# Optimization experiments

Hardware: AMD Instinct MI355X
Metric: run time of the kernel (lower is better)

## Reference

```python
import jax, jax.numpy as jnp
import numpy as np

B, N, D, K = 256, 500000, 64, 100


def setup_inputs() -> dict:
    key = jax.random.key(0)
    k1, k2, k3 = jax.random.split(key, 3)
    query_embedding = jax.random.normal(k1, (B, D), dtype=jnp.float32)
    corpus = jax.random.normal(k2, (N, D), dtype=jnp.float32)
    corpus_id = jax.random.randint(k3, (N,), 0, 10_000_000).astype(jnp.int64)
    return {
        "query_embedding": query_embedding,
        "corpus": corpus,
        "corpus_id": corpus_id,
        "num_items": K,
    }


def reference(query_embedding, corpus, corpus_id, num_items):
    # Inner-product scores: [B, N]
    scores = jnp.matmul(query_embedding, corpus.T)
    # Top-k along the corpus axis (lax.top_k returns sorted descending,
    # matching torch.topk defaults): values [B, k], indices [B, k]
    inprod_scores, indices = jax.lax.top_k(scores, num_items)
    # Gather ids and embeddings of the neighbors
    item_ids = corpus_id[indices]          # [B, k]
    embeddings = corpus[indices]           # [B, k, D]
    return (item_ids, inprod_scores, embeddings)
```

## Files before the change

kernel.cpp:

```cpp
#include <hip/hip_runtime.h>
#include <math.h>

#define NQ      256
#define DIM     64
#define NCORPUS 500000
#define K       100
#define CAP     2048
#define ZTHRESH 3.0f

#define NSUB    16
#define SUBCAP  160
#define TILE    32
#define NTILES  (NCORPUS / TILE)
#define K1BLOCKS 1024

typedef __bf16 bf16x8 __attribute__((ext_vector_type(8)));
typedef float  f32x16 __attribute__((ext_vector_type(16)));

static __device__ __forceinline__ bf16x8 pack8(float4 a, float4 b) {
    bf16x8 r;
    r[0] = (__bf16)a.x; r[1] = (__bf16)a.y; r[2] = (__bf16)a.z; r[3] = (__bf16)a.w;
    r[4] = (__bf16)b.x; r[5] = (__bf16)b.y; r[6] = (__bf16)b.z; r[7] = (__bf16)b.w;
    return r;
}

__global__ void k0_setup(const float* __restrict__ q, int* __restrict__ cnt2,
                         float* __restrict__ t) {
    int b = threadIdx.x;
    const float4* qb = (const float4*)(q + b * DIM);
    float s = 0.f;
#pragma unroll
    for (int i = 0; i < DIM / 4; ++i) {
        float4 v = qb[i];
        s += v.x * v.x + v.y * v.y + v.z * v.z + v.w * v.w;
    }
    t[b] = ZTHRESH * sqrtf(s);
    for (int i = b; i < NQ * NSUB * 4; i += 256) cnt2[i] = 0;
}

__global__ __launch_bounds__(256, 4)
void k1_score_filter(const float* __restrict__ q, const float* __restrict__ c,
                     const float* __restrict__ t, int* __restrict__ cnt2,
                     int* __restrict__ cand2) {
    const int tid  = threadIdx.x;
    const int ln   = tid & 63;
    const int lm   = ln & 31;
    const int half = ln >> 5;

    __shared__ __align__(16) __bf16 qf[2048 * 8];

#pragma unroll
    for (int u = 0; u < 8; ++u) {
        const int ch = u * 256 + tid;
        const int ci = ch >> 8;
        const int cs = (ch >> 6) & 3;
        const int cl = ch & 63;
        const float* src =
            q + ((ci << 5) + (cl & 31)) * DIM + cs * 16 + ((cl >> 5) << 3);
        float4 a = *(const float4*)src;
        float4 b = *(const float4*)(src + 4);
        *(bf16x8*)(qf + (size_t)ch * 8) = pack8(a, b);
    }
    __syncthreads();

    float tq[8];
#pragma unroll
    for (int i = 0; i < 8; ++i) tq[i] = t[(i << 5) + lm];

    const f32x16 z16 = {0, 0, 0, 0, 0, 0, 0, 0, 0, 0, 0, 0, 0, 0, 0, 0};

    const int wid    = (blockIdx.x << 2) | (tid >> 6);
    const int stride = gridDim.x << 2;
    const int sub    = wid & (NSUB - 1);

    float4 st[8];
#define LOADC(tl)                                                             \
    {                                                                         \
        const float* gp = c + (size_t)((tl) * TILE + lm) * DIM + (half << 3); \
        _Pragma("unroll") for (int s = 0; s < 4; ++s) {                       \
            st[2 * s]     = *(const float4*)(gp + s * 16);                    \
            st[2 * s + 1] = *(const float4*)(gp + s * 16 + 4);                \
        }                                                                     \
    }
    LOADC(wid);

    for (int tl = wid; tl < NTILES; tl += stride) {
        float4 cur[8];
#pragma unroll
        for (int s = 0; s < 8; ++s) cur[s] = st[s];
        const int nx = tl + stride;
        if (nx < NTILES) LOADC(nx);
        bf16x8 af[4];
#pragma unroll
        for (int s = 0; s < 4; ++s) af[s] = pack8(cur[2 * s], cur[2 * s + 1]);

        for (int i = 0; i < 8; ++i) {
            const __bf16* bp = qf + ((size_t)(i << 2) * 64 + ln) * 8;
            bf16x8 b0 = *(const bf16x8*)(bp);
            bf16x8 b1 = *(const bf16x8*)(bp + 512);
            bf16x8 b2 = *(const bf16x8*)(bp + 1024);
            bf16x8 b3 = *(const bf16x8*)(bp + 1536);
            f32x16 acc;
            acc = __builtin_amdgcn_mfma_f32_32x32x16_bf16(af[0], b0, z16, 0, 0, 0);
            acc = __builtin_amdgcn_mfma_f32_32x32x16_bf16(af[1], b1, acc, 0, 0, 0);
            acc = __builtin_amdgcn_mfma_f32_32x32x16_bf16(af[2], b2, acc, 0, 0, 0);
            acc = __builtin_amdgcn_mfma_f32_32x32x16_bf16(af[3], b3, acc, 0, 0, 0);
            float mx = acc[0];
#pragma unroll
            for (int r = 1; r < 16; ++r) mx = fmaxf(mx, acc[r]);
            const float ti = tq[i];
            if (__any(mx > ti)) {
                const int qidx = (i << 5) + lm;
                const int rowb = tl * TILE + (half << 2);
#pragma unroll
                for (int r = 0; r < 16; ++r) {
                    if (acc[r] > ti) {
                        int slot = atomicAdd(&cnt2[(qidx * NSUB + sub) * 4], 1);
                        if (slot < SUBCAP)
                            cand2[(size_t)(qidx * NSUB + sub) * SUBCAP + slot] =
                                rowb + (r & 3) + ((r >> 2) << 3);
                    }
                }
            }
        }
    }
#undef LOADC
}

__global__ __launch_bounds__(512) void k2_select(
    const float* __restrict__ q, const float* __restrict__ c,
    const int* __restrict__ ids, const int* __restrict__ cnt2,
    const int* __restrict__ cand2, float* __restrict__ out) {
    const int b = blockIdx.x;
    const int tid = threadIdx.x;
    __shared__ double qd[DIM];
    __shared__ int pref[NSUB + 1];
    __shared__ int clist[CAP];
    __shared__ unsigned long long keys[CAP];
    __shared__ int sidx[K];

    if (tid < DIM) qd[tid] = (double)q[b * DIM + tid];
    if (tid == 0) {
        int a = 0;
        for (int s = 0; s < NSUB; ++s) {
            pref[s] = a;
            int cs = cnt2[(b * NSUB + s) * 4];
            if (cs > SUBCAP) cs = SUBCAP;
            a += cs;
            if (a > CAP) a = CAP;
        }
        pref[NSUB] = a;
    }
    __syncthreads();
#pragma unroll
    for (int s = 0; s < NSUB; ++s) {
        const int base = pref[s];
        const int cs = pref[s + 1] - base;
        for (int i = tid; i < cs; i += 512)
            clist[base + i] = cand2[(size_t)(b * NSUB + s) * SUBCAP + i];
    }
    __syncthreads();
    const int n = pref[NSUB];
    int p = 128;
    while (p < n) p <<= 1;

    for (int i = tid; i < p; i += 512) {
        unsigned long long key = 0ull;
        if (i < n) {
            const int idx = clist[i];
            const float4* cr = (const float4*)(c + (size_t)idx * DIM);
            double acc = 0.0;
#pragma unroll
            for (int d4 = 0; d4 < DIM / 4; ++d4) {
                float4 v = cr[d4];
                acc += qd[4 * d4 + 0] * (double)v.x;
                acc += qd[4 * d4 + 1] * (double)v.y;
                acc += qd[4 * d4 + 2] * (double)v.z;
                acc += qd[4 * d4 + 3] * (double)v.w;
            }
            const float sc = (float)acc;
            unsigned u = __float_as_uint(sc);
            u = (u & 0x80000000u) ? ~u : (u | 0x80000000u);
            key = ((unsigned long long)u << 32) | (unsigned)(~(unsigned)idx);
        }
        keys[i] = key;
    }
    __syncthreads();

    for (int kk = 2; kk <= p; kk <<= 1) {
        for (int j = kk >> 1; j > 0; j >>= 1) {
            for (int i = tid; i < p; i += 512) {
                const int l = i ^ j;
                if (l > i) {
                    const unsigned long long a = keys[i], bb = keys[l];
                    const bool desc = ((i & kk) == 0);
                    if (desc ? (a < bb) : (a > bb)) {
                        keys[i] = bb;
                        keys[l] = a;
                    }
                }
            }
            __syncthreads();
        }
    }

    if (tid < K) {
        const unsigned long long key = keys[tid];
        const unsigned uk = (unsigned)(key >> 32);
        const unsigned us = (uk & 0x80000000u) ? (uk & 0x7fffffffu) : ~uk;
        int idx = (int)(~(unsigned)(key & 0xffffffffu));
        if ((unsigned)idx >= NCORPUS) idx = 0;
        sidx[tid] = idx;
        out[b * K + tid] = (float)ids[idx];
        out[NQ * K + b * K + tid] = __uint_as_float(us);
    }
    __syncthreads();
    for (int e = tid; e < K * DIM; e += 512) {
        const int j = e >> 6;
        const int d = e & 63;
        out[2 * NQ * K + (size_t)b * K * DIM + e] = c[(size_t)sidx[j] * DIM + d];
    }
}

extern "C" void kernel_launch(void* const* d_in, const int* in_sizes, int n_in,
                              void* d_out, int out_size, void* d_ws,
                              size_t ws_size, hipStream_t stream) {
    const float* q = (const float*)d_in[0];
    const float* c = (const float*)d_in[1];
    const int* ids = (const int*)d_in[2];
    float* out = (float*)d_out;

    char* ws = (char*)d_ws;
    float* t   = (float*)ws;
    int* cnt2  = (int*)(ws + 4096);
    int* cand2 = (int*)(ws + 4096 + 65536);

    k0_setup<<<1, 256, 0, stream>>>(q, cnt2, t);
    k1_score_filter<<<K1BLOCKS, 256, 0, stream>>>(q, c, t, cnt2, cand2);
    k2_select<<<NQ, 512, 0, stream>>>(q, c, ids, cnt2, cand2, out);
}
```

Baseline: 270.3 us.

## Stage corpus tiles via async global-to-LDS triple buffering and batch candidate atomics

The scoring kernel now streams corpus tiles into a per-wave triple-buffered LDS region using global_load_lds with swizzled offsets and explicit vmcnt waits, replacing the register-held prefetch. Grid size drops to 256 blocks, and the occupancy hint is removed. Candidates are first appended to a per-wave LDS queue and flushed to the global per-query buckets at the end, which cuts global atomics during the main loop. The risks are lower occupancy from the large LDS footprint and silently dropped candidates if a wave's queue exceeds its capacity of 320.

```diff
diff --git a/kernel.cpp b/kernel.cpp
--- a/kernel.cpp
+++ b/kernel.cpp
@@ -1,5 +1,6 @@
 #include <hip/hip_runtime.h>
 #include <math.h>
+#include <stdint.h>
 
 #define NQ      256
 #define DIM     64
@@ -12,10 +13,16 @@
 #define SUBCAP  160
 #define TILE    32
 #define NTILES  (NCORPUS / TILE)
-#define K1BLOCKS 1024
+#define K1BLOCKS 256
+#define NWAVE1  (K1BLOCKS * 4)
+#define WQCAP   320
 
 typedef __bf16 bf16x8 __attribute__((ext_vector_type(8)));
 typedef float  f32x16 __attribute__((ext_vector_type(16)));
+typedef __attribute__((address_space(3))) unsigned       lds_u32;
+typedef const __attribute__((address_space(1))) unsigned glb_u32;
+
+#define WAITVM(N) __builtin_amdgcn_s_waitcnt(((N) & 0xF) | (((N) >> 4) << 14) | 0x0F70)
 
 static __device__ __forceinline__ bf16x8 pack8(float4 a, float4 b) {
     bf16x8 r;
@@ -38,7 +45,7 @@
     for (int i = b; i < NQ * NSUB * 4; i += 256) cnt2[i] = 0;
 }
 
-__global__ __launch_bounds__(256, 4)
+__global__ __launch_bounds__(256)
 void k1_score_filter(const float* __restrict__ q, const float* __restrict__ c,
                      const float* __restrict__ t, int* __restrict__ cnt2,
                      int* __restrict__ cand2) {
@@ -46,8 +53,14 @@
     const int ln   = tid & 63;
     const int lm   = ln & 31;
     const int half = ln >> 5;
+    const int wv   = tid >> 6;
 
     __shared__ __align__(16) __bf16 qf[2048 * 8];
+    __shared__ __align__(16) char   cbuf[4 * 3 * 8192];
+    __shared__ unsigned wq[4 * WQCAP];
+    __shared__ int wqc[4 * 16];
+
+    if (ln == 0) wqc[wv * 16] = 0;
 
 #pragma unroll
     for (int u = 0; u < 8; ++u) {
@@ -67,32 +80,64 @@
 #pragma unroll
     for (int i = 0; i < 8; ++i) tq[i] = t[(i << 5) + lm];
 
+    int offs[8];
+#pragma unroll
+    for (int g = 0; g < 8; ++g) {
+        int r = g * 4 + (ln >> 4);
+        int j = (ln & 15) ^ (r & 15);
+        offs[g] = r * 256 + j * 16;
+    }
+    int roff[8];
+#pragma unroll
+    for (int s = 0; s < 4; ++s) {
+        int c0 = s * 4 + half * 2;
+#pragma unroll
+        for (int tt = 0; tt < 2; ++tt)
+            roff[s * 2 + tt] = lm * 256 + ((((c0 + tt) ^ (lm & 15))) << 4);
+    }
+
+    char* cbase = cbuf + wv * 3 * 8192;
+    const int wid = (blockIdx.x << 2) | wv;
+    const int sub = wid & (NSUB - 1);
+
+    WAITVM(0);
+
+#define STAGE(tl, bi)                                                         \
+    {                                                                         \
+        const char* gb = (const char*)c + (size_t)(tl) * 8192;                \
+        char* lb = cbase + (bi) * 8192;                                       \
+        _Pragma("unroll") for (int g = 0; g < 8; ++g)                         \
+            __builtin_amdgcn_global_load_lds(                                 \
+                (glb_u32*)(uintptr_t)(gb + offs[g]),                          \
+                (lds_u32*)(uintptr_t)(lb + g * 1024), 16, 0, 0);              \
+    }
+
+    STAGE(wid, 0);
+    STAGE(wid + NWAVE1, 1);
+
     const f32x16 z16 = {0, 0, 0, 0, 0, 0, 0, 0, 0, 0, 0, 0, 0, 0, 0, 0};
-
-    const int wid    = (blockIdx.x << 2) | (tid >> 6);
-    const int stride = gridDim.x << 2;
-    const int sub    = wid & (NSUB - 1);
-
-    float4 st[8];
-#define LOADC(tl)                                                             \
-    {                                                                         \
-        const float* gp = c + (size_t)((tl) * TILE + lm) * DIM + (half << 3); \
-        _Pragma("unroll") for (int s = 0; s < 4; ++s) {                       \
-            st[2 * s]     = *(const float4*)(gp + s * 16);                    \
-            st[2 * s + 1] = *(const float4*)(gp + s * 16 + 4);                \
-        }                                                                     \
-    }
-    LOADC(wid);
-
-    for (int tl = wid; tl < NTILES; tl += stride) {
-        float4 cur[8];
-#pragma unroll
-        for (int s = 0; s < 8; ++s) cur[s] = st[s];
-        const int nx = tl + stride;
-        if (nx < NTILES) LOADC(nx);
+    int bi = 0;
+    for (int tl = wid; tl < NTILES; tl += NWAVE1) {
+        const int nx2 = tl + 2 * NWAVE1;
+        if (nx2 < NTILES) {
+            int b2 = bi + 2;
+            if (b2 >= 3) b2 -= 3;
+            STAGE(nx2, b2);
+            WAITVM(16);
+        } else if (tl + NWAVE1 < NTILES) {
+            WAITVM(8);
+        } else {
+            WAITVM(0);
+        }
+
+        const char* tb = cbase + bi * 8192;
         bf16x8 af[4];
 #pragma unroll
-        for (int s = 0; s < 4; ++s) af[s] = pack8(cur[2 * s], cur[2 * s + 1]);
+        for (int s = 0; s < 4; ++s) {
+            float4 u = *(const float4*)(tb + roff[2 * s]);
+            float4 v = *(const float4*)(tb + roff[2 * s + 1]);
+            af[s] = pack8(u, v);
+        }
 
         for (int i = 0; i < 8; ++i) {
             const __bf16* bp = qf + ((size_t)(i << 2) * 64 + ln) * 8;
@@ -110,21 +155,35 @@
             for (int r = 1; r < 16; ++r) mx = fmaxf(mx, acc[r]);
             const float ti = tq[i];
             if (__any(mx > ti)) {
-                const int qidx = (i << 5) + lm;
+                const unsigned qidx = (unsigned)((i << 5) + lm);
                 const int rowb = tl * TILE + (half << 2);
 #pragma unroll
                 for (int r = 0; r < 16; ++r) {
                     if (acc[r] > ti) {
-                        int slot = atomicAdd(&cnt2[(qidx * NSUB + sub) * 4], 1);
-                        if (slot < SUBCAP)
-                            cand2[(size_t)(qidx * NSUB + sub) * SUBCAP + slot] =
-                                rowb + (r & 3) + ((r >> 2) << 3);
+                        int pos = atomicAdd(&wqc[wv * 16], 1);
+                        if (pos < WQCAP)
+                            wq[wv * WQCAP + pos] =
+                                (qidx << 19) |
+                                (unsigned)(rowb + (r & 3) + ((r >> 2) << 3));
                     }
                 }
             }
         }
-    }
-#undef LOADC
+        bi += 1;
+        if (bi == 3) bi = 0;
+    }
+#undef STAGE
+
+    int cw = wqc[wv * 16];
+    if (cw > WQCAP) cw = WQCAP;
+    for (int kx = ln; kx < cw; kx += 64) {
+        unsigned e = wq[wv * WQCAP + kx];
+        int qidx = (int)(e >> 19);
+        int row  = (int)(e & 0x7FFFFu);
+        int slot = atomicAdd(&cnt2[(qidx * NSUB + sub) * 4], 1);
+        if (slot < SUBCAP)
+            cand2[(size_t)(qidx * NSUB + sub) * SUBCAP + slot] = row;
+    }
 }
 
 __global__ __launch_bounds__(512) void k2_select(
```

New measurement: 286.2 us. 5.9% more time.

## Double-buffer corpus loads with inline asm and stage candidates in LDS

Applied to the files above, without the earlier changes.

Replaces the compiler-scheduled prefetch with two explicit register buffers filled by inline-asm global_load_dwordx4 and explicit vmcnt waits. This keeps one tile's loads in flight while the previous tile is computed. Candidate hits are also appended to a per-wave LDS queue and flushed to the global per-query atomic counters only at the end, which avoids global atomics inside the hot loop. The risks are that the per-wave queue cap of 160 can silently drop candidates when a wave sees many hits, and that the hand-written waitcnt logic is fragile.

```diff
diff --git a/kernel.cpp b/kernel.cpp
--- a/kernel.cpp
+++ b/kernel.cpp
@@ -1,5 +1,6 @@
 #include <hip/hip_runtime.h>
 #include <math.h>
+#include <stdint.h>
 
 #define NQ      256
 #define DIM     64
@@ -13,9 +14,15 @@
 #define TILE    32
 #define NTILES  (NCORPUS / TILE)
 #define K1BLOCKS 1024
+#define NWAVE1  (K1BLOCKS * 4)
+#define WQCAP   160
 
 typedef __bf16 bf16x8 __attribute__((ext_vector_type(8)));
 typedef float  f32x16 __attribute__((ext_vector_type(16)));
+
+#define SB() __builtin_amdgcn_sched_barrier(0)
+#define WAITVM_B(N) \
+    __builtin_amdgcn_s_waitcnt(((N) & 0xF) | (((N) >> 4) << 14) | 0x0F70)
 
 static __device__ __forceinline__ bf16x8 pack8(float4 a, float4 b) {
     bf16x8 r;
@@ -37,6 +44,31 @@
     t[b] = ZTHRESH * sqrtf(s);
     for (int i = b; i < NQ * NSUB * 4; i += 256) cnt2[i] = 0;
 }
+
+#define LOADT(d0, d1, d2, d3, d4, d5, d6, d7, tl)                             \
+    {                                                                         \
+        const char* gp_ = (const char*)c +                                    \
+                          ((size_t)(tl) * TILE + lm) * 256 + (half << 5);     \
+        asm volatile(                                                         \
+            "global_load_dwordx4 %0, %[a], off\n\t"                           \
+            "global_load_dwordx4 %1, %[a], off offset:16\n\t"                 \
+            "global_load_dwordx4 %2, %[a], off offset:64\n\t"                 \
+            "global_load_dwordx4 %3, %[a], off offset:80\n\t"                 \
+            "global_load_dwordx4 %4, %[a], off offset:128\n\t"                \
+            "global_load_dwordx4 %5, %[a], off offset:144\n\t"                \
+            "global_load_dwordx4 %6, %[a], off offset:192\n\t"                \
+            "global_load_dwordx4 %7, %[a], off offset:208\n\t"                \
+            : "=&v"(d0), "=&v"(d1), "=&v"(d2), "=&v"(d3),                     \
+              "=&v"(d4), "=&v"(d5), "=&v"(d6), "=&v"(d7)                      \
+            : [a] "v"(gp_));                                                  \
+    }
+
+#define WAITASM(N)                                                            \
+    do {                                                                      \
+        SB();                                                                 \
+        asm volatile("s_waitcnt vmcnt(" #N ")" ::: "memory");                 \
+        SB();                                                                 \
+    } while (0)
 
 __global__ __launch_bounds__(256, 4)
 void k1_score_filter(const float* __restrict__ q, const float* __restrict__ c,
@@ -46,8 +78,13 @@
     const int ln   = tid & 63;
     const int lm   = ln & 31;
     const int half = ln >> 5;
+    const int wv   = tid >> 6;
 
     __shared__ __align__(16) __bf16 qf[2048 * 8];
+    __shared__ unsigned wq[4 * WQCAP];
+    __shared__ int wqc[4 * 16];
+
+    if (ln == 0) wqc[wv * 16] = 0;
 
 #pragma unroll
     for (int u = 0; u < 8; ++u) {
@@ -66,65 +103,94 @@
     float tq[8];
 #pragma unroll
     for (int i = 0; i < 8; ++i) tq[i] = t[(i << 5) + lm];
-
+    SB();
+    WAITVM_B(0);
+    SB();
+
+    const int wid = (blockIdx.x << 2) | wv;
+    const int sub = wid & (NSUB - 1);
     const f32x16 z16 = {0, 0, 0, 0, 0, 0, 0, 0, 0, 0, 0, 0, 0, 0, 0, 0};
 
-    const int wid    = (blockIdx.x << 2) | (tid >> 6);
-    const int stride = gridDim.x << 2;
-    const int sub    = wid & (NSUB - 1);
-
-    float4 st[8];
-#define LOADC(tl)                                                             \
+#define COMPUTE(s0, s1, s2, s3, s4, s5, s6, s7, tl)                           \
     {                                                                         \
-        const float* gp = c + (size_t)((tl) * TILE + lm) * DIM + (half << 3); \
-        _Pragma("unroll") for (int s = 0; s < 4; ++s) {                       \
-            st[2 * s]     = *(const float4*)(gp + s * 16);                    \
-            st[2 * s + 1] = *(const float4*)(gp + s * 16 + 4);                \
+        bf16x8 af0 = pack8(s0, s1), af1 = pack8(s2, s3);                      \
+        bf16x8 af2 = pack8(s4, s5), af3 = pack8(s6, s7);                      \
+        for (int i = 0; i < 8; ++i) {                                         \
+            const __bf16* bp = qf + ((size_t)(i << 2) * 64 + ln) * 8;         \
+            bf16x8 b0 = *(const bf16x8*)(bp);                                 \
+            bf16x8 b1 = *(const bf16x8*)(bp + 512);                           \
+            bf16x8 b2 = *(const bf16x8*)(bp + 1024);                          \
+            bf16x8 b3 = *(const bf16x8*)(bp + 1536);                          \
+            f32x16 acc;                                                       \
+            acc = __builtin_amdgcn_mfma_f32_32x32x16_bf16(af0, b0, z16,       \
+                                                          0, 0, 0);           \
+            acc = __builtin_amdgcn_mfma_f32_32x32x16_bf16(af1, b1, acc,       \
+                                                          0, 0, 0);           \
+            acc = __builtin_amdgcn_mfma_f32_32x32x16_bf16(af2, b2, acc,       \
+                                                          0, 0, 0);           \
+            acc = __builtin_amdgcn_mfma_f32_32x32x16_bf16(af3, b3, acc,       \
+                                                          0, 0, 0);           \
+            const float ti = tq[i];                                           \
+            float mx = acc[0];                                                \
+            _Pragma("unroll") for (int r = 1; r < 16; ++r)                    \
+                mx = fmaxf(mx, acc[r]);                                       \
+            if (__any(mx > ti)) {                                             \
+                const unsigned qidx = (unsigned)((i << 5) + lm);              \
+                const int rowb = (tl) * TILE + (half << 2);                   \
+                _Pragma("unroll") for (int r = 0; r < 16; ++r) {              \
+                    if (acc[r] > ti) {                                        \
+                        int pos = atomicAdd(&wqc[wv * 16], 1);                \
+                        if (pos < WQCAP)                                      \
+                            wq[wv * WQCAP + pos] =                            \
+                                (qidx << 19) |                                \
+                                (unsigned)(rowb + (r & 3) + ((r >> 2) << 3)); \
+                    }                                                         \
+                }                                                             \
+            }                                                                 \
         }                                                                     \
     }
-    LOADC(wid);
-
-    for (int tl = wid; tl < NTILES; tl += stride) {
-        float4 cur[8];
-#pragma unroll
-        for (int s = 0; s < 8; ++s) cur[s] = st[s];
-        const int nx = tl + stride;
-        if (nx < NTILES) LOADC(nx);
-        bf16x8 af[4];
-#pragma unroll
-        for (int s = 0; s < 4; ++s) af[s] = pack8(cur[2 * s], cur[2 * s + 1]);
-
-        for (int i = 0; i < 8; ++i) {
-            const __bf16* bp = qf + ((size_t)(i << 2) * 64 + ln) * 8;
-            bf16x8 b0 = *(const bf16x8*)(bp);
-            bf16x8 b1 = *(const bf16x8*)(bp + 512);
-            bf16x8 b2 = *(const bf16x8*)(bp + 1024);
-            bf16x8 b3 = *(const bf16x8*)(bp + 1536);
-            f32x16 acc;
-            acc = __builtin_amdgcn_mfma_f32_32x32x16_bf16(af[0], b0, z16, 0, 0, 0);
-            acc = __builtin_amdgcn_mfma_f32_32x32x16_bf16(af[1], b1, acc, 0, 0, 0);
-            acc = __builtin_amdgcn_mfma_f32_32x32x16_bf16(af[2], b2, acc, 0, 0, 0);
-            acc = __builtin_amdgcn_mfma_f32_32x32x16_bf16(af[3], b3, acc, 0, 0, 0);
-            float mx = acc[0];
-#pragma unroll
-            for (int r = 1; r < 16; ++r) mx = fmaxf(mx, acc[r]);
-            const float ti = tq[i];
-            if (__any(mx > ti)) {
-                const int qidx = (i << 5) + lm;
-                const int rowb = tl * TILE + (half << 2);
-#pragma unroll
-                for (int r = 0; r < 16; ++r) {
-                    if (acc[r] > ti) {
-                        int slot = atomicAdd(&cnt2[(qidx * NSUB + sub) * 4], 1);
-                        if (slot < SUBCAP)
-                            cand2[(size_t)(qidx * NSUB + sub) * SUBCAP + slot] =
-                                rowb + (r & 3) + ((r >> 2) << 3);
-                    }
-                }
-            }
-        }
-    }
-#undef LOADC
+
+    float4 a0, a1, a2, a3, a4, a5, a6, a7;
+    float4 b0_, b1_, b2_, b3_, b4_, b5_, b6_, b7_;
+    int tl = wid;
+    LOADT(a0, a1, a2, a3, a4, a5, a6, a7, tl);
+    for (;;) {
+        int tn = tl + NWAVE1;
+        if (tn < NTILES) {
+            LOADT(b0_, b1_, b2_, b3_, b4_, b5_, b6_, b7_, tn);
+            WAITASM(8);
+        } else {
+            WAITASM(0);
+        }
+        COMPUTE(a0, a1, a2, a3, a4, a5, a6, a7, tl);
+        if (tn >= NTILES) break;
+        tl = tn;
+        tn = tl + NWAVE1;
+        if (tn < NTILES) {
+            LOADT(a0, a1, a2, a3, a4, a5, a6, a7, tn);
+            WAITASM(8);
+        } else {
+            WAITASM(0);
+        }
+        COMPUTE(b0_, b1_, b2_, b3_, b4_, b5_, b6_, b7_, tl);
+        if (tn >= NTILES) break;
+        tl = tn;
+    }
+#undef COMPUTE
+
+    SB();
+    WAITVM_B(0);
+    SB();
+    int cw = wqc[wv * 16];
+    if (cw > WQCAP) cw = WQCAP;
+    for (int kx = ln; kx < cw; kx += 64) {
+        unsigned e = wq[wv * WQCAP + kx];
+        int qidx = (int)(e >> 19);
+        int row  = (int)(e & 0x7FFFFu);
+        int slot = atomicAdd(&cnt2[(qidx * NSUB + sub) * 4], 1);
+        if (slot < SUBCAP)
+            cand2[(size_t)(qidx * NSUB + sub) * SUBCAP + slot] = row;
+    }
 }
 
 __global__ __launch_bounds__(512) void k2_select(
```

Measured after the change: 255.4 us. 5.5% less time.

## Stage corpus tiles in LDS via async loads and split queries across waves

Applied to the files above, without the earlier changes.

The scoring kernel now keeps each wave's 64 queries in registers as bf16 fragments and loads 64-row corpus tiles into double-buffered, XOR-swizzled LDS with global_load_lds. All four waves share each tile, so corpus reads and MFMA work are divided by query instead of by corpus tile. Threshold hits go first into a per-wave LDS queue and are flushed to global candidate lists once, after the loop, replacing per-hit global atomics. The per-wave queue is capped at 160 entries, so extra hits are silently dropped, which could lose true top-k candidates. The tile count is also hardcoded, with clamping on the last partial tile.

```diff
diff --git a/kernel.cpp b/kernel.cpp
--- a/kernel.cpp
+++ b/kernel.cpp
@@ -1,5 +1,6 @@
 #include <hip/hip_runtime.h>
 #include <math.h>
+#include <stdint.h>
 
 #define NQ      256
 #define DIM     64
@@ -10,12 +11,15 @@
 
 #define NSUB    16
 #define SUBCAP  160
-#define TILE    32
-#define NTILES  (NCORPUS / TILE)
+#define TILE64  64
+#define NT64    7813
 #define K1BLOCKS 1024
+#define WQCAP   160
 
 typedef __bf16 bf16x8 __attribute__((ext_vector_type(8)));
 typedef float  f32x16 __attribute__((ext_vector_type(16)));
+typedef __attribute__((address_space(3))) unsigned       lds_u32;
+typedef const __attribute__((address_space(1))) unsigned glb_u32;
 
 static __device__ __forceinline__ bf16x8 pack8(float4 a, float4 b) {
     bf16x8 r;
@@ -46,85 +50,126 @@
     const int ln   = tid & 63;
     const int lm   = ln & 31;
     const int half = ln >> 5;
-
-    __shared__ __align__(16) __bf16 qf[2048 * 8];
-
-#pragma unroll
-    for (int u = 0; u < 8; ++u) {
-        const int ch = u * 256 + tid;
-        const int ci = ch >> 8;
-        const int cs = (ch >> 6) & 3;
-        const int cl = ch & 63;
-        const float* src =
-            q + ((ci << 5) + (cl & 31)) * DIM + cs * 16 + ((cl >> 5) << 3);
-        float4 a = *(const float4*)src;
-        float4 b = *(const float4*)(src + 4);
-        *(bf16x8*)(qf + (size_t)ch * 8) = pack8(a, b);
-    }
-    __syncthreads();
-
-    float tq[8];
-#pragma unroll
-    for (int i = 0; i < 8; ++i) tq[i] = t[(i << 5) + lm];
+    const int wv   = tid >> 6;
+
+    __shared__ __align__(16) float cstage[2][TILE64 * DIM];
+    __shared__ unsigned wq[4 * WQCAP];
+    __shared__ int wqc[4 * 16];
+
+    if (ln == 0) wqc[wv * 16] = 0;
+
+    const int qbase = wv << 6;
+    bf16x8 bf[2][4];
+    float tq[2];
+#pragma unroll
+    for (int nt = 0; nt < 2; ++nt) {
+        const float* qr = q + (qbase + (nt << 5) + lm) * DIM;
+#pragma unroll
+        for (int s = 0; s < 4; ++s) {
+            float4 u = *(const float4*)(qr + s * 16 + (half << 3));
+            float4 v = *(const float4*)(qr + s * 16 + (half << 3) + 4);
+            bf[nt][s] = pack8(u, v);
+        }
+        tq[nt] = t[qbase + (nt << 5) + lm];
+    }
+
+#define STAGE(tl, b)                                                          \
+    {                                                                         \
+        _Pragma("unroll") for (int g = 0; g < 4; ++g) {                       \
+            const int rl = (wv << 4) + (g << 2) + (ln >> 4);                  \
+            int row = (tl) * TILE64 + rl;                                     \
+            if (row > NCORPUS - 1) row = NCORPUS - 1;         \
+            const int ch = (ln & 15) ^ (rl & 15);                             \
+            const char* gp =                                                  \
+                (const char*)c + (size_t)row * 256 + (ch << 4);               \
+            char* lp = (char*)&cstage[b][(size_t)(((wv << 4) + (g << 2))      \
+                                                  << 6)];                     \
+            __builtin_amdgcn_global_load_lds((glb_u32*)(uintptr_t)gp,         \
+                                             (lds_u32*)(uintptr_t)lp, 16, 0,  \
+                                             0);                              \
+        }                                                                     \
+    }
 
     const f32x16 z16 = {0, 0, 0, 0, 0, 0, 0, 0, 0, 0, 0, 0, 0, 0, 0, 0};
 
-    const int wid    = (blockIdx.x << 2) | (tid >> 6);
-    const int stride = gridDim.x << 2;
-    const int sub    = wid & (NSUB - 1);
-
-    float4 st[8];
-#define LOADC(tl)                                                             \
+#define COMPUTE(b, tl)                                                        \
     {                                                                         \
-        const float* gp = c + (size_t)((tl) * TILE + lm) * DIM + (half << 3); \
-        _Pragma("unroll") for (int s = 0; s < 4; ++s) {                       \
-            st[2 * s]     = *(const float4*)(gp + s * 16);                    \
-            st[2 * s + 1] = *(const float4*)(gp + s * 16 + 4);                \
+        bf16x8 af[2][4];                                                      \
+        _Pragma("unroll") for (int a = 0; a < 2; ++a) {                       \
+            const char* rb =                                                  \
+                (const char*)&cstage[b][(size_t)(((a << 5) + lm) << 6)];      \
+            _Pragma("unroll") for (int s = 0; s < 4; ++s) {                   \
+                const int c0 = (s << 2) + (half << 1);                        \
+                float4 u =                                                    \
+                    *(const float4*)(rb + ((c0 ^ (lm & 15)) << 4));           \
+                float4 v =                                                    \
+                    *(const float4*)(rb + (((c0 + 1) ^ (lm & 15)) << 4));     \
+                af[a][s] = pack8(u, v);                                       \
+            }                                                                 \
         }                                                                     \
-    }
-    LOADC(wid);
-
-    for (int tl = wid; tl < NTILES; tl += stride) {
-        float4 cur[8];
-#pragma unroll
-        for (int s = 0; s < 8; ++s) cur[s] = st[s];
-        const int nx = tl + stride;
-        if (nx < NTILES) LOADC(nx);
-        bf16x8 af[4];
-#pragma unroll
-        for (int s = 0; s < 4; ++s) af[s] = pack8(cur[2 * s], cur[2 * s + 1]);
-
-        for (int i = 0; i < 8; ++i) {
-            const __bf16* bp = qf + ((size_t)(i << 2) * 64 + ln) * 8;
-            bf16x8 b0 = *(const bf16x8*)(bp);
-            bf16x8 b1 = *(const bf16x8*)(bp + 512);
-            bf16x8 b2 = *(const bf16x8*)(bp + 1024);
-            bf16x8 b3 = *(const bf16x8*)(bp + 1536);
-            f32x16 acc;
-            acc = __builtin_amdgcn_mfma_f32_32x32x16_bf16(af[0], b0, z16, 0, 0, 0);
-            acc = __builtin_amdgcn_mfma_f32_32x32x16_bf16(af[1], b1, acc, 0, 0, 0);
-            acc = __builtin_amdgcn_mfma_f32_32x32x16_bf16(af[2], b2, acc, 0, 0, 0);
-            acc = __builtin_amdgcn_mfma_f32_32x32x16_bf16(af[3], b3, acc, 0, 0, 0);
-            float mx = acc[0];
-#pragma unroll
-            for (int r = 1; r < 16; ++r) mx = fmaxf(mx, acc[r]);
-            const float ti = tq[i];
-            if (__any(mx > ti)) {
-                const int qidx = (i << 5) + lm;
-                const int rowb = tl * TILE + (half << 2);
-#pragma unroll
-                for (int r = 0; r < 16; ++r) {
-                    if (acc[r] > ti) {
-                        int slot = atomicAdd(&cnt2[(qidx * NSUB + sub) * 4], 1);
-                        if (slot < SUBCAP)
-                            cand2[(size_t)(qidx * NSUB + sub) * SUBCAP + slot] =
-                                rowb + (r & 3) + ((r >> 2) << 3);
-                    }
-                }
-            }
-        }
-    }
-#undef LOADC
+        _Pragma("unroll") for (int a = 0; a < 2; ++a) {                       \
+            _Pragma("unroll") for (int nt = 0; nt < 2; ++nt) {                \
+                f32x16 acc;                                                   \
+                acc = __builtin_amdgcn_mfma_f32_32x32x16_bf16(                \
+                    af[a][0], bf[nt][0], z16, 0, 0, 0);                       \
+                acc = __builtin_amdgcn_mfma_f32_32x32x16_bf16(                \
+                    af[a][1], bf[nt][1], acc, 0, 0, 0);                       \
+                acc = __builtin_amdgcn_mfma_f32_32x32x16_bf16(                \
+                    af[a][2], bf[nt][2], acc, 0, 0, 0);                       \
+                acc = __builtin_amdgcn_mfma_f32_32x32x16_bf16(                \
+                    af[a][3], bf[nt][3], acc, 0, 0, 0);                       \
+                const float ti = tq[nt];                                      \
+                float mx = acc[0];                                            \
+                _Pragma("unroll") for (int r = 1; r < 16; ++r)                \
+                    mx = fmaxf(mx, acc[r]);                                   \
+                if (__any(mx > ti)) {                                         \
+                    const unsigned qidx =                                     \
+                        (unsigned)(qbase + (nt << 5) + lm);                   \
+                    const int rowb = (tl) * TILE64 + (a << 5) + (half << 2);  \
+                    _Pragma("unroll") for (int r = 0; r < 16; ++r) {          \
+                        if (acc[r] > ti) {                                    \
+                            const int row =                                   \
+                                rowb + (r & 3) + ((r >> 2) << 3);             \
+                            if (row < NCORPUS) {               \
+                                int pos = atomicAdd(&wqc[wv * 16], 1);        \
+                                if (pos < WQCAP)                              \
+                                    wq[wv * WQCAP + pos] =                    \
+                                        (qidx << 19) | (unsigned)row;         \
+                            }                                                 \
+                        }                                                     \
+                    }                                                         \
+                }                                                             \
+            }                                                                 \
+        }                                                                     \
+    }
+
+    int tl = blockIdx.x;
+    int buf = 0;
+    STAGE(tl, 0);
+    for (;;) {
+        const int tn = tl + K1BLOCKS;
+        if (tn < NT64) STAGE(tn, buf ^ 1);
+        __syncthreads();
+        COMPUTE(buf, tl);
+        if (tn >= NT64) break;
+        __syncthreads();
+        buf ^= 1;
+        tl = tn;
+    }
+#undef COMPUTE
+#undef STAGE
+
+    const int sub = blockIdx.x & (NSUB - 1);
+    int cw = wqc[wv * 16];
+    if (cw > WQCAP) cw = WQCAP;
+    for (int kx = ln; kx < cw; kx += 64) {
+        unsigned e = wq[wv * WQCAP + kx];
+        int qidx = (int)(e >> 19);
+        int row  = (int)(e & 0x7FFFFu);
+        int slot = atomicAdd(&cnt2[(qidx * NSUB + sub) * 4], 1);
+        if (slot < SUBCAP)
+            cand2[(size_t)(qidx * NSUB + sub) * SUBCAP + slot] = row;
+    }
 }
 
 __global__ __launch_bounds__(512) void k2_select(
```

New measurement: 248.4 us. -8.1%, faster.
